# Kernel optimization log

Hardware: AMD Instinct MI355X
Metric: run time of the kernel (lower is better)

## Reference

```python
import jax, jax.numpy as jnp
import numpy as np

N_NODES = 100000
N_EDGES = 1600000
IN_CH = 6
EDGE_FEAT = 8


def glorot(key, shape):
    lim = np.sqrt(6.0 / (shape[0] + shape[1]))
    return jax.random.uniform(key, shape, jnp.float32, -lim, lim)


def setup_inputs() -> dict:
    key = jax.random.key(0)
    ks = jax.random.split(key, 10)
    x = jax.random.normal(ks[0], (N_NODES, IN_CH), jnp.float32)
    edge_index = jax.random.randint(ks[1], (2, N_EDGES), 0, N_NODES, jnp.int64)
    edge_attr = jax.random.normal(ks[2], (N_EDGES, EDGE_FEAT), jnp.float32)
    return {
        "x": x,
        "edge_index": edge_index,
        "edge_attr": edge_attr,
        "W1": glorot(ks[3], (IN_CH, 32)), "b1": jnp.zeros((32,), jnp.float32),
        "W2": glorot(ks[4], (32, 16)), "b2": jnp.zeros((16,), jnp.float32),
        "W3": glorot(ks[5], (16 * 2 + EDGE_FEAT, 32)), "b3": jnp.zeros((32,), jnp.float32),
        "W4": glorot(ks[6], (32, 1)), "b4": jnp.zeros((1,), jnp.float32),
    }


def gcn_conv(x, src, dst, W, b, n_nodes):
    # PyG GCNConv: add self-loops, symmetric deg^{-1/2} normalization,
    # linear transform, scatter-add aggregation over incoming edges, bias.
    h = x @ W  # [N, out]
    deg = jnp.zeros((n_nodes,), h.dtype).at[dst].add(1.0) + 1.0  # +1 self-loop
    dinv = jax.lax.rsqrt(deg)  # [N]
    norm = dinv[src] * dinv[dst]  # [E]
    msg = h[src] * norm[:, None]  # gather + scale
    agg = jnp.zeros_like(h).at[dst].add(msg)
    agg = agg + h * (dinv * dinv)[:, None]  # self-loop term
    return agg + b


def reference(x, edge_index, edge_attr, W1, b1, W2, b2, W3, b3, W4, b4):
    src, dst = edge_index[0], edge_index[1]
    n = x.shape[0]
    h = jax.nn.relu(gcn_conv(x, src, dst, W1, b1, n))
    h = jax.nn.relu(gcn_conv(h, src, dst, W2, b2, n))
    # edge gather-concat-MLP
    edge_input = jnp.concatenate([h[src], h[dst], edge_attr], axis=1)  # [E, 40]
    out = jax.nn.relu(edge_input @ W3 + b3) @ W4 + b4  # [E, 1]
    return out.squeeze(-1)
```

## Files before the change

### kernel.cpp

```cpp
#include <hip/hip_runtime.h>


constexpr int TPB = 256;
constexpr int NB = 256;
constexpr int BSH = 8;
constexpr int MAXB = 1024;
constexpr int EDGE_ITERS = 4;

using short8  = __attribute__((ext_vector_type(8))) short;
using f32x4   = __attribute__((ext_vector_type(4))) float;
using uintx4  = __attribute__((ext_vector_type(4))) unsigned;
using floatx4 = __attribute__((ext_vector_type(4))) float;

__device__ __forceinline__ void nt_store4(uint4 v, uint4* p) {
    uintx4 e = {v.x, v.y, v.z, v.w};
    __builtin_nontemporal_store(e, reinterpret_cast<uintx4*>(p));
}
__device__ __forceinline__ float4 nt_load_f4(const float4* p) {
    floatx4 e = __builtin_nontemporal_load(reinterpret_cast<const floatx4*>(p));
    return float4{e.x, e.y, e.z, e.w};
}

__device__ __forceinline__ float bf_lo(unsigned w) {
    return __builtin_bit_cast(float, (unsigned)(w << 16));
}
__device__ __forceinline__ float bf_hi(unsigned w) {
    return __builtin_bit_cast(float, w & 0xFFFF0000u);
}
__device__ __forceinline__ unsigned bf1(float f) {
    unsigned u = __builtin_bit_cast(unsigned, f);
    return (u + 0x7FFFu + ((u >> 16) & 1u)) >> 16;
}
__device__ __forceinline__ unsigned pk(float lo, float hi) {
    return bf1(lo) | (bf1(hi) << 16);
}
__device__ __forceinline__ void unp8(uint4 v, float* o) {
    o[0] = bf_lo(v.x); o[1] = bf_hi(v.x); o[2] = bf_lo(v.y); o[3] = bf_hi(v.y);
    o[4] = bf_lo(v.z); o[5] = bf_hi(v.z); o[6] = bf_lo(v.w); o[7] = bf_hi(v.w);
}
__device__ __forceinline__ void unp6(uint4 v, float* o) {
    o[0] = bf_lo(v.x); o[1] = bf_hi(v.x); o[2] = bf_lo(v.y); o[3] = bf_hi(v.y);
    o[4] = bf_lo(v.z); o[5] = bf_hi(v.z);
}

__global__ void k_bhist(const int* __restrict__ dst, unsigned* __restrict__ histG,
                        int E, int B, int CH) {
    __shared__ unsigned h[MAXB];
    for (int t = threadIdx.x; t < B; t += blockDim.x) h[t] = 0;
    __syncthreads();
    int b = blockIdx.x;
    int beg = b * CH, end = min(E, beg + CH);
    for (int i = beg + threadIdx.x; i < end; i += blockDim.x)
        atomicAdd(&h[__builtin_nontemporal_load(dst + i) >> BSH], 1u);
    __syncthreads();
    for (int t = threadIdx.x; t < B; t += blockDim.x) histG[b * B + t] = h[t];
}

__global__ void k_scan1t(const unsigned* __restrict__ histG, unsigned* __restrict__ bsum,
                         int M, int B) {
    __shared__ unsigned s[TPB];
    int tid = threadIdx.x;
    int i = blockIdx.x * TPB + tid;
    unsigned v = (i < M) ? histG[(i % NB) * B + (i / NB)] : 0u;
    s[tid] = v;
    __syncthreads();
    for (int ofs = TPB / 2; ofs > 0; ofs >>= 1) {
        if (tid < ofs) s[tid] += s[tid + ofs];
        __syncthreads();
    }
    if (tid == 0) bsum[blockIdx.x] = s[0];
}

__global__ void k_scan2(unsigned* __restrict__ bsum, int nb) {
    __shared__ unsigned s[512];
    int tid = threadIdx.x;
    unsigned v = (tid < nb) ? bsum[tid] : 0u;
    s[tid] = v;
    __syncthreads();
    for (int ofs = 1; ofs < 512; ofs <<= 1) {
        unsigned t = (tid >= ofs) ? s[tid - ofs] : 0u;
        __syncthreads();
        s[tid] += t;
        __syncthreads();
    }
    if (tid < nb) bsum[tid] = s[tid] - v;
}

__global__ void k_scan3t(const unsigned* __restrict__ histG, const unsigned* __restrict__ bsum,
                         unsigned* __restrict__ scannedM, int M, int B) {
    __shared__ unsigned s[TPB];
    int tid = threadIdx.x;
    int i = blockIdx.x * TPB + tid;
    unsigned v = (i < M) ? histG[(i % NB) * B + (i / NB)] : 0u;
    s[tid] = v;
    __syncthreads();
    for (int ofs = 1; ofs < TPB; ofs <<= 1) {
        unsigned t = (tid >= ofs) ? s[tid - ofs] : 0u;
        __syncthreads();
        s[tid] += t;
        __syncthreads();
    }
    if (i < M) scannedM[i] = bsum[blockIdx.x] + s[tid] - v;
}

__global__ void k_bscatter(const int* __restrict__ src, const int* __restrict__ dst,
                           const unsigned* __restrict__ scannedM, unsigned* __restrict__ lvl1,
                           int E, int B, int CH) {
    __shared__ unsigned cur[MAXB];
    int b = blockIdx.x;
    for (int t = threadIdx.x; t < B; t += blockDim.x) cur[t] = scannedM[t * NB + b];
    __syncthreads();
    int beg = b * CH, end = min(E, beg + CH);
    for (int i = beg + threadIdx.x; i < end; i += blockDim.x) {
        int d = __builtin_nontemporal_load(dst + i);
        int sv = __builtin_nontemporal_load(src + i);
        int bk = d >> BSH;
        unsigned p = atomicAdd(&cur[bk], 1u);
        lvl1[p] = ((unsigned)sv << BSH) | (unsigned)(d & ((1 << BSH) - 1));
    }
}

__global__ void k_bbuild(const unsigned* __restrict__ lvl1, const unsigned* __restrict__ scannedM,
                         const float* __restrict__ x, unsigned* __restrict__ rowptr,
                         float* __restrict__ dinv, uint4* __restrict__ xs,
                         int* __restrict__ csr_src, int N, int E, int B) {
    __shared__ unsigned cnt[1 << BSH];
    __shared__ unsigned ro[1 << BSH];
    int b = blockIdx.x;
    int tid = threadIdx.x;
    unsigned gbase = scannedM[(size_t)b * NB];
    unsigned gend = (b + 1 < B) ? scannedM[(size_t)(b + 1) * NB] : (unsigned)E;
    cnt[tid] = 0;
    __syncthreads();
    for (unsigned i = gbase + tid; i < gend; i += (unsigned)blockDim.x)
        atomicAdd(&cnt[lvl1[i] & ((1u << BSH) - 1u)], 1u);
    __syncthreads();
    unsigned v = cnt[tid];
    ro[tid] = v;
    __syncthreads();
    for (int ofs = 1; ofs < (1 << BSH); ofs <<= 1) {
        unsigned t = (tid >= ofs) ? ro[tid - ofs] : 0u;
        __syncthreads();
        ro[tid] += t;
        __syncthreads();
    }
    unsigned excl = ro[tid] - v;
    int n = (b << BSH) + tid;
    if (n < N) {
        rowptr[n] = gbase + excl;
        float di = rsqrtf((float)v + 1.0f);
        dinv[n] = di;
        const float* xr = x + (size_t)n * 6;
        uint4 o;
        o.x = pk(xr[0] * di, xr[1] * di);
        o.y = pk(xr[2] * di, xr[3] * di);
        o.z = pk(xr[4] * di, xr[5] * di);
        o.w = 0u;
        xs[n] = o;
        if (n == N - 1) rowptr[N] = gend;
    }
    __syncthreads();
    cnt[tid] = gbase + excl;
    __syncthreads();
    for (unsigned i = gbase + tid; i < gend; i += (unsigned)blockDim.x) {
        unsigned w = lvl1[i];
        unsigned p = atomicAdd(&cnt[w & ((1u << BSH) - 1u)], 1u);
        csr_src[p] = (int)(w >> BSH);
    }
}

__global__ void k_gagg6f(const unsigned* __restrict__ rowptr, const int* __restrict__ csr_src,
                         const float* __restrict__ dinv, const uint4* __restrict__ xs,
                         const float* __restrict__ W1, const float* __restrict__ b1,
                         const float* __restrict__ W2, uint4* __restrict__ hs2, int N) {
    int gid = blockIdx.x * blockDim.x + threadIdx.x;
    int n = gid >> 2, q = gid & 3;
    if (n >= N) return;
    unsigned beg = rowptr[n], end = rowptr[n + 1];
    float acc[6] = {0.f, 0.f, 0.f, 0.f, 0.f, 0.f};
    for (unsigned j = beg + q; j < end; j += 4) {
        int s = __builtin_nontemporal_load(csr_src + j);
        float t[6];
        unp6(xs[s], t);
#pragma unroll
        for (int i = 0; i < 6; ++i) acc[i] += t[i];
    }
#pragma unroll
    for (int i = 0; i < 6; ++i) {
        acc[i] += __shfl_xor(acc[i], 1);
        acc[i] += __shfl_xor(acc[i], 2);
    }
    float t6[6];
    unp6(xs[n], t6);
#pragma unroll
    for (int i = 0; i < 6; ++i) acc[i] += t6[i];
    float di = dinv[n];
    float h1[8];
#pragma unroll
    for (int cc = 0; cc < 8; ++cc) {
        int oc = q * 8 + cc;
        float s = 0.f;
#pragma unroll
        for (int k = 0; k < 6; ++k) s = fmaf(acc[k], W1[k * 32 + oc], s);
        h1[cc] = fmaxf(fmaf(s, di, b1[oc]), 0.f);
    }
    float z[16];
#pragma unroll
    for (int j = 0; j < 16; ++j) z[j] = 0.f;
#pragma unroll
    for (int cc = 0; cc < 8; ++cc) {
        int c = q * 8 + cc;
        float a = h1[cc];
#pragma unroll
        for (int j = 0; j < 16; ++j) z[j] = fmaf(a, W2[c * 16 + j], z[j]);
    }
#pragma unroll
    for (int j = 0; j < 16; ++j) {
        z[j] += __shfl_xor(z[j], 1);
        z[j] += __shfl_xor(z[j], 2);
    }
    if (q < 2) {
        unsigned w[4];
#pragma unroll
        for (int p = 0; p < 4; ++p)
            w[p] = pk(z[q * 8 + 2 * p] * di, z[q * 8 + 2 * p + 1] * di);
        nt_store4(uint4{w[0], w[1], w[2], w[3]}, hs2 + (size_t)n * 2 + q);
    }
}

__global__ void k_gagg16(const unsigned* __restrict__ rowptr, const int* __restrict__ csr_src,
                         const float* __restrict__ dinv, const uint4* __restrict__ hs2,
                         const float* __restrict__ b2, uint4* __restrict__ h2, int N) {
    int gid = blockIdx.x * blockDim.x + threadIdx.x;
    int n = gid >> 3, q = gid & 7;
    int h = q & 1, e4 = q >> 1;
    if (n >= N) return;
    unsigned beg = rowptr[n], end = rowptr[n + 1];
    float acc[8] = {0.f, 0.f, 0.f, 0.f, 0.f, 0.f, 0.f, 0.f};
    for (unsigned j = beg + e4; j < end; j += 4) {
        int s = __builtin_nontemporal_load(csr_src + j);
        float t[8];
        unp8(hs2[(size_t)s * 2 + h], t);
#pragma unroll
        for (int i = 0; i < 8; ++i) acc[i] += t[i];
    }
#pragma unroll
    for (int i = 0; i < 8; ++i) {
        acc[i] += __shfl_xor(acc[i], 2);
        acc[i] += __shfl_xor(acc[i], 4);
    }
    if (e4) return;
    float t8[8];
    unp8(hs2[(size_t)n * 2 + h], t8);
    float di = dinv[n];
    unsigned w[4];
#pragma unroll
    for (int i = 0; i < 4; ++i) {
        float r0 = fmaxf(fmaf(acc[2 * i] + t8[2 * i], di, b2[h * 8 + 2 * i]), 0.f);
        float r1 = fmaxf(fmaf(acc[2 * i + 1] + t8[2 * i + 1], di, b2[h * 8 + 2 * i + 1]), 0.f);
        w[i] = pk(r0, r1);
    }
    h2[(size_t)n * 2 + h] = uint4{w[0], w[1], w[2], w[3]};
}

__global__ void k_wprep(const float* __restrict__ W3, const float* __restrict__ b3,
                        uint4* __restrict__ w3tab) {
    int lane = threadIdx.x;
    if (lane >= 64) return;
    int l15 = lane & 15, kb = lane >> 4;
    unsigned w0[2][4], w1[2][4];
#pragma unroll
    for (int t = 0; t < 2; ++t) {
#pragma unroll
        for (int p = 0; p < 4; ++p) {
            int k0 = kb * 8 + 2 * p;
            w0[t][p] = pk(W3[k0 * 32 + t * 16 + l15], W3[(k0 + 1) * 32 + t * 16 + l15]);
            int k1 = 32 + kb * 8 + 2 * p;
            float f0 = (k1 < 40) ? W3[k1 * 32 + t * 16 + l15]
                                 : (k1 == 40 ? b3[t * 16 + l15] : 0.f);
            float f1 = (k1 + 1 < 40) ? W3[(k1 + 1) * 32 + t * 16 + l15] : 0.f;
            w1[t][p] = pk(f0, f1);
        }
    }
    w3tab[lane * 4 + 0] = uint4{w0[0][0], w0[0][1], w0[0][2], w0[0][3]};
    w3tab[lane * 4 + 1] = uint4{w0[1][0], w0[1][1], w0[1][2], w0[1][3]};
    w3tab[lane * 4 + 2] = uint4{w1[0][0], w1[0][1], w1[0][2], w1[0][3]};
    w3tab[lane * 4 + 3] = uint4{w1[1][0], w1[1][1], w1[1][2], w1[1][3]};
}

__global__ void __launch_bounds__(TPB) k_edge_mfma(
    const int* __restrict__ src, const int* __restrict__ dst,
    const uint4* __restrict__ h2, const float* __restrict__ eattr,
    const uint4* __restrict__ w3tab, const float* __restrict__ W4,
    const float* __restrict__ b4, float* __restrict__ out, int E) {
    const int lane = threadIdx.x & 63;
    const int wave = threadIdx.x >> 6;
    const int l15 = lane & 15;
    const int kb = lane >> 4;

    short8 w3k0[2], w3k1[2];
    {
        const uint4* wt = w3tab + (size_t)lane * 4;
        w3k0[0] = __builtin_bit_cast(short8, wt[0]);
        w3k0[1] = __builtin_bit_cast(short8, wt[1]);
        w3k1[0] = __builtin_bit_cast(short8, wt[2]);
        w3k1[1] = __builtin_bit_cast(short8, wt[3]);
    }
    const float4 w4v0 = reinterpret_cast<const float4*>(W4)[kb];
    const float4 w4v1 = reinterpret_cast<const float4*>(W4)[4 + kb];
    const float b4v = b4[0];
    const int* idx_tab = (kb >= 2) ? dst : src;
    const long base0 = ((long)blockIdx.x * 4 + wave) * (16L * EDGE_ITERS);

    const uint4 one_u = (kb == 1) ? uint4{0x3F80u, 0u, 0u, 0u} : uint4{0u, 0u, 0u, 0u};
    const short8 one_s8 = __builtin_bit_cast(short8, one_u);

    auto eclamp = [&](int it) -> size_t {
        long et = base0 + (long)it * 16 + l15;
        return (size_t)(et < E ? et : (long)(E - 1));
    };
    auto load_a1 = [&](int it) -> short8 {
        if (kb != 0) return one_s8;
        const float4* ea = reinterpret_cast<const float4*>(eattr + eclamp(it) * 8);
        float4 e0 = nt_load_f4(ea);
        float4 e1 = nt_load_f4(ea + 1);
        return __builtin_bit_cast(short8, uint4{pk(e0.x, e0.y), pk(e0.z, e0.w),
                                                pk(e1.x, e1.y), pk(e1.z, e1.w)});
    };

    int idx[EDGE_ITERS];
#pragma unroll
    for (int it = 0; it < EDGE_ITERS; ++it)
        idx[it] = __builtin_nontemporal_load(idx_tab + eclamp(it));

    uint4 hvA = h2[(size_t)idx[0] * 2 + (kb & 1)];
    short8 a1A = load_a1(0);
    uint4 hvB = h2[(size_t)idx[1] * 2 + (kb & 1)];
    short8 a1B = load_a1(1);

#pragma unroll
    for (int it = 0; it < EDGE_ITERS; ++it) {
        uint4 hvC{0u, 0u, 0u, 0u};
        short8 a1C = one_s8;
        if (it + 2 < EDGE_ITERS) {
            hvC = h2[(size_t)idx[it + 2] * 2 + (kb & 1)];
            a1C = load_a1(it + 2);
        }

        short8 a0 = __builtin_bit_cast(short8, hvA);
        f32x4 c0 = {0.f, 0.f, 0.f, 0.f}, c1 = {0.f, 0.f, 0.f, 0.f};
        c0 = __builtin_amdgcn_mfma_f32_16x16x32_bf16(w3k0[0], a0, c0, 0, 0, 0);
        c0 = __builtin_amdgcn_mfma_f32_16x16x32_bf16(w3k1[0], a1A, c0, 0, 0, 0);
        c1 = __builtin_amdgcn_mfma_f32_16x16x32_bf16(w3k0[1], a0, c1, 0, 0, 0);
        c1 = __builtin_amdgcn_mfma_f32_16x16x32_bf16(w3k1[1], a1A, c1, 0, 0, 0);

        float z = fmaxf(c0[0], 0.f) * w4v0.x;
        z = fmaf(fmaxf(c0[1], 0.f), w4v0.y, z);
        z = fmaf(fmaxf(c0[2], 0.f), w4v0.z, z);
        z = fmaf(fmaxf(c0[3], 0.f), w4v0.w, z);
        z = fmaf(fmaxf(c1[0], 0.f), w4v1.x, z);
        z = fmaf(fmaxf(c1[1], 0.f), w4v1.y, z);
        z = fmaf(fmaxf(c1[2], 0.f), w4v1.z, z);
        z = fmaf(fmaxf(c1[3], 0.f), w4v1.w, z);
        z += __shfl_xor(z, 16);
        z += __shfl_xor(z, 32);
        long erow = base0 + (long)it * 16 + l15;
        if (kb == 0 && erow < E) __builtin_nontemporal_store(z + b4v, out + erow);

        hvA = hvB; a1A = a1B;
        hvB = hvC; a1B = a1C;
    }
}

extern "C" void kernel_launch(void* const* d_in, const int* in_sizes, int n_in,
                              void* d_out, int out_size, void* d_ws, size_t ws_size,
                              hipStream_t stream) {
    const float* x     = (const float*)d_in[0];
    const int*   ei    = (const int*)d_in[1];
    const float* eattr = (const float*)d_in[2];
    const float* W1 = (const float*)d_in[3];
    const float* b1 = (const float*)d_in[4];
    const float* W2 = (const float*)d_in[5];
    const float* b2 = (const float*)d_in[6];
    const float* W3 = (const float*)d_in[7];
    const float* b3 = (const float*)d_in[8];
    const float* W4 = (const float*)d_in[9];
    const float* b4 = (const float*)d_in[10];
    float* out = (float*)d_out;

    const int N = in_sizes[0] / 6;
    const int E = in_sizes[2] / 8;
    const int* src = ei;
    const int* dst = ei + E;

    const int B  = (N + (1 << BSH) - 1) >> BSH;
    const int CH = (E + NB - 1) / NB;
    const int M  = B * NB;
    const int nbM = (M + TPB - 1) / TPB;

    char* wsb = (char*)d_ws;
    size_t off = 0;
    auto alloc4 = [&](size_t elems) {
        void* p = wsb + off;
        off += ((elems * 4 + 15) & ~(size_t)15);
        return p;
    };
    unsigned* rowptr   = (unsigned*)alloc4(N + 1);
    float*    dinv     = (float*)alloc4(N);
    unsigned* bsum     = (unsigned*)alloc4(512);
    unsigned* histG    = (unsigned*)alloc4((size_t)NB * B);
    unsigned* scannedM = (unsigned*)alloc4((size_t)NB * B);
    int*      csr_src  = (int*)alloc4(E);
    unsigned* big      = (unsigned*)alloc4((size_t)N * 16 > (size_t)E ? (size_t)N * 16 : (size_t)E);
    uint4*    xs       = (uint4*)alloc4((size_t)N * 4);
    uint4*    w3tab    = (uint4*)alloc4(64 * 4 * 4);

    unsigned* lvl1 = big;
    uint4*    hs2  = (uint4*)big;
    uint4*    h2   = (uint4*)(big + (size_t)N * 8);

    k_wprep<<<1, 64, 0, stream>>>(W3, b3, w3tab);

    k_bhist   <<<NB, TPB, 0, stream>>>(dst, histG, E, B, CH);
    k_scan1t  <<<nbM, TPB, 0, stream>>>(histG, bsum, M, B);
    k_scan2   <<<1, 512, 0, stream>>>(bsum, nbM);
    k_scan3t  <<<nbM, TPB, 0, stream>>>(histG, bsum, scannedM, M, B);
    k_bscatter<<<NB, TPB, 0, stream>>>(src, dst, scannedM, lvl1, E, B, CH);
    k_bbuild  <<<B, 1 << BSH, 0, stream>>>(lvl1, scannedM, x, rowptr, dinv, xs, csr_src, N, E, B);

    k_gagg6f<<<((size_t)N * 4 + TPB - 1) / TPB, TPB, 0, stream>>>(
        rowptr, csr_src, dinv, xs, W1, b1, W2, hs2, N);

    k_gagg16<<<((size_t)N * 8 + TPB - 1) / TPB, TPB, 0, stream>>>(
        rowptr, csr_src, dinv, hs2, b2, h2, N);

    const long per_block = 4L * 16 * EDGE_ITERS;
    const int eblocks = (int)((E + per_block - 1) / per_block);
    k_edge_mfma<<<eblocks, TPB, 0, stream>>>(src, dst, (const uint4*)h2, eattr,
                                             (const uint4*)w3tab, W4, b4, out, E);
}
```

Baseline: 178.2 us.

## Switch edge MLP to 32x32x16 MFMA processing 32 edges per wave

Reworks the edge MLP so each wave handles 32 edges per iteration with three 32x32x16 bf16 MFMAs (src features, dst features, edge attrs plus bias) instead of four 16x16x32 MFMAs over 16 edges. The weight table is repacked into three K-slices per lane, and the W4 reduction now needs only one cross-lane shuffle. This halves the number of blocks, amortises index and weight setup over more edges and cuts shuffles. In exchange each lane issues two gathers per iteration (src and dst) and holds a 16-wide accumulator, which raises register pressure.

```diff
diff --git a/kernel.cpp b/kernel.cpp
--- a/kernel.cpp
+++ b/kernel.cpp
@@ -8,7 +8,7 @@
 constexpr int EDGE_ITERS = 4;
 
 using short8  = __attribute__((ext_vector_type(8))) short;
-using f32x4   = __attribute__((ext_vector_type(4))) float;
+using f32x16  = __attribute__((ext_vector_type(16))) float;
 using uintx4  = __attribute__((ext_vector_type(4))) unsigned;
 using floatx4 = __attribute__((ext_vector_type(4))) float;
 
@@ -267,25 +267,19 @@
                         uint4* __restrict__ w3tab) {
     int lane = threadIdx.x;
     if (lane >= 64) return;
-    int l15 = lane & 15, kb = lane >> 4;
-    unsigned w0[2][4], w1[2][4];
-#pragma unroll
-    for (int t = 0; t < 2; ++t) {
+    int j = lane & 31, hi = lane >> 5;
+#pragma unroll
+    for (int s = 0; s < 3; ++s) {
+        unsigned w[4];
 #pragma unroll
         for (int p = 0; p < 4; ++p) {
-            int k0 = kb * 8 + 2 * p;
-            w0[t][p] = pk(W3[k0 * 32 + t * 16 + l15], W3[(k0 + 1) * 32 + t * 16 + l15]);
-            int k1 = 32 + kb * 8 + 2 * p;
-            float f0 = (k1 < 40) ? W3[k1 * 32 + t * 16 + l15]
-                                 : (k1 == 40 ? b3[t * 16 + l15] : 0.f);
-            float f1 = (k1 + 1 < 40) ? W3[(k1 + 1) * 32 + t * 16 + l15] : 0.f;
-            w1[t][p] = pk(f0, f1);
+            int k0 = s * 16 + hi * 8 + 2 * p;
+            float f0 = (k0 < 40) ? W3[k0 * 32 + j] : (k0 == 40 ? b3[j] : 0.f);
+            float f1 = (k0 + 1 < 40) ? W3[(k0 + 1) * 32 + j] : 0.f;
+            w[p] = pk(f0, f1);
         }
-    }
-    w3tab[lane * 4 + 0] = uint4{w0[0][0], w0[0][1], w0[0][2], w0[0][3]};
-    w3tab[lane * 4 + 1] = uint4{w0[1][0], w0[1][1], w0[1][2], w0[1][3]};
-    w3tab[lane * 4 + 2] = uint4{w1[0][0], w1[0][1], w1[0][2], w1[0][3]};
-    w3tab[lane * 4 + 3] = uint4{w1[1][0], w1[1][1], w1[1][2], w1[1][3]};
+        w3tab[lane * 3 + s] = uint4{w[0], w[1], w[2], w[3]};
+    }
 }
 
 __global__ void __launch_bounds__(TPB) k_edge_mfma(
@@ -295,32 +289,30 @@
     const float* __restrict__ b4, float* __restrict__ out, int E) {
     const int lane = threadIdx.x & 63;
     const int wave = threadIdx.x >> 6;
-    const int l15 = lane & 15;
-    const int kb = lane >> 4;
-
-    short8 w3k0[2], w3k1[2];
+    const int e31 = lane & 31;
+    const int hi = lane >> 5;
+
+    short8 wA0, wA1, wA2;
     {
-        const uint4* wt = w3tab + (size_t)lane * 4;
-        w3k0[0] = __builtin_bit_cast(short8, wt[0]);
-        w3k0[1] = __builtin_bit_cast(short8, wt[1]);
-        w3k1[0] = __builtin_bit_cast(short8, wt[2]);
-        w3k1[1] = __builtin_bit_cast(short8, wt[3]);
-    }
-    const float4 w4v0 = reinterpret_cast<const float4*>(W4)[kb];
-    const float4 w4v1 = reinterpret_cast<const float4*>(W4)[4 + kb];
+        const uint4* wt = w3tab + (size_t)lane * 3;
+        wA0 = __builtin_bit_cast(short8, wt[0]);
+        wA1 = __builtin_bit_cast(short8, wt[1]);
+        wA2 = __builtin_bit_cast(short8, wt[2]);
+    }
+    const float4* W4v = reinterpret_cast<const float4*>(W4);
+    const float4 w4q0 = W4v[hi], w4q1 = W4v[2 + hi], w4q2 = W4v[4 + hi], w4q3 = W4v[6 + hi];
     const float b4v = b4[0];
-    const int* idx_tab = (kb >= 2) ? dst : src;
-    const long base0 = ((long)blockIdx.x * 4 + wave) * (16L * EDGE_ITERS);
-
-    const uint4 one_u = (kb == 1) ? uint4{0x3F80u, 0u, 0u, 0u} : uint4{0u, 0u, 0u, 0u};
+    const long base0 = ((long)blockIdx.x * 4 + wave) * (32L * EDGE_ITERS);
+
+    const uint4 one_u = (hi == 1) ? uint4{0x3F80u, 0u, 0u, 0u} : uint4{0u, 0u, 0u, 0u};
     const short8 one_s8 = __builtin_bit_cast(short8, one_u);
 
     auto eclamp = [&](int it) -> size_t {
-        long et = base0 + (long)it * 16 + l15;
+        long et = base0 + (long)it * 32 + e31;
         return (size_t)(et < E ? et : (long)(E - 1));
     };
-    auto load_a1 = [&](int it) -> short8 {
-        if (kb != 0) return one_s8;
+    auto load_a2 = [&](int it) -> short8 {
+        if (hi != 0) return one_s8;
         const float4* ea = reinterpret_cast<const float4*>(eattr + eclamp(it) * 8);
         float4 e0 = nt_load_f4(ea);
         float4 e1 = nt_load_f4(ea + 1);
@@ -328,47 +320,49 @@
                                                 pk(e1.x, e1.y), pk(e1.z, e1.w)});
     };
 
-    int idx[EDGE_ITERS];
-#pragma unroll
-    for (int it = 0; it < EDGE_ITERS; ++it)
-        idx[it] = __builtin_nontemporal_load(idx_tab + eclamp(it));
-
-    uint4 hvA = h2[(size_t)idx[0] * 2 + (kb & 1)];
-    short8 a1A = load_a1(0);
-    uint4 hvB = h2[(size_t)idx[1] * 2 + (kb & 1)];
-    short8 a1B = load_a1(1);
-
+    int is[EDGE_ITERS], id[EDGE_ITERS];
 #pragma unroll
     for (int it = 0; it < EDGE_ITERS; ++it) {
-        uint4 hvC{0u, 0u, 0u, 0u};
-        short8 a1C = one_s8;
+        is[it] = __builtin_nontemporal_load(src + eclamp(it));
+        id[it] = __builtin_nontemporal_load(dst + eclamp(it));
+    }
+
+    uint4 hsA = h2[(size_t)is[0] * 2 + hi], hdA = h2[(size_t)id[0] * 2 + hi];
+    short8 a2A = load_a2(0);
+    uint4 hsB = h2[(size_t)is[1] * 2 + hi], hdB = h2[(size_t)id[1] * 2 + hi];
+    short8 a2B = load_a2(1);
+
+#pragma unroll
+    for (int it = 0; it < EDGE_ITERS; ++it) {
+        uint4 hsC{0u, 0u, 0u, 0u}, hdC{0u, 0u, 0u, 0u};
+        short8 a2C = one_s8;
         if (it + 2 < EDGE_ITERS) {
-            hvC = h2[(size_t)idx[it + 2] * 2 + (kb & 1)];
-            a1C = load_a1(it + 2);
+            hsC = h2[(size_t)is[it + 2] * 2 + hi];
+            hdC = h2[(size_t)id[it + 2] * 2 + hi];
+            a2C = load_a2(it + 2);
         }
 
-        short8 a0 = __builtin_bit_cast(short8, hvA);
-        f32x4 c0 = {0.f, 0.f, 0.f, 0.f}, c1 = {0.f, 0.f, 0.f, 0.f};
-        c0 = __builtin_amdgcn_mfma_f32_16x16x32_bf16(w3k0[0], a0, c0, 0, 0, 0);
-        c0 = __builtin_amdgcn_mfma_f32_16x16x32_bf16(w3k1[0], a1A, c0, 0, 0, 0);
-        c1 = __builtin_amdgcn_mfma_f32_16x16x32_bf16(w3k0[1], a0, c1, 0, 0, 0);
-        c1 = __builtin_amdgcn_mfma_f32_16x16x32_bf16(w3k1[1], a1A, c1, 0, 0, 0);
-
-        float z = fmaxf(c0[0], 0.f) * w4v0.x;
-        z = fmaf(fmaxf(c0[1], 0.f), w4v0.y, z);
-        z = fmaf(fmaxf(c0[2], 0.f), w4v0.z, z);
-        z = fmaf(fmaxf(c0[3], 0.f), w4v0.w, z);
-        z = fmaf(fmaxf(c1[0], 0.f), w4v1.x, z);
-        z = fmaf(fmaxf(c1[1], 0.f), w4v1.y, z);
-        z = fmaf(fmaxf(c1[2], 0.f), w4v1.z, z);
-        z = fmaf(fmaxf(c1[3], 0.f), w4v1.w, z);
-        z += __shfl_xor(z, 16);
+        f32x16 c;
+#pragma unroll
+        for (int i = 0; i < 16; ++i) c[i] = 0.f;
+        c = __builtin_amdgcn_mfma_f32_32x32x16_bf16(wA0, __builtin_bit_cast(short8, hsA), c, 0, 0, 0);
+        c = __builtin_amdgcn_mfma_f32_32x32x16_bf16(wA1, __builtin_bit_cast(short8, hdA), c, 0, 0, 0);
+        c = __builtin_amdgcn_mfma_f32_32x32x16_bf16(wA2, a2A, c, 0, 0, 0);
+
+        float z = 0.f;
+#pragma unroll
+        for (int r = 0; r < 4; ++r) {
+            z = fmaf(fmaxf(c[0 * 4 + r], 0.f), ((const float*)&w4q0)[r], z);
+            z = fmaf(fmaxf(c[1 * 4 + r], 0.f), ((const float*)&w4q1)[r], z);
+            z = fmaf(fmaxf(c[2 * 4 + r], 0.f), ((const float*)&w4q2)[r], z);
+            z = fmaf(fmaxf(c[3 * 4 + r], 0.f), ((const float*)&w4q3)[r], z);
+        }
         z += __shfl_xor(z, 32);
-        long erow = base0 + (long)it * 16 + l15;
-        if (kb == 0 && erow < E) __builtin_nontemporal_store(z + b4v, out + erow);
-
-        hvA = hvB; a1A = a1B;
-        hvB = hvC; a1B = a1C;
+        long erow = base0 + (long)it * 32 + e31;
+        if (hi == 0 && erow < E) __builtin_nontemporal_store(z + b4v, out + erow);
+
+        hsA = hsB; hdA = hdB; a2A = a2B;
+        hsB = hsC; hdB = hdC; a2B = a2C;
     }
 }
 
@@ -413,7 +407,7 @@
     int*      csr_src  = (int*)alloc4(E);
     unsigned* big      = (unsigned*)alloc4((size_t)N * 16 > (size_t)E ? (size_t)N * 16 : (size_t)E);
     uint4*    xs       = (uint4*)alloc4((size_t)N * 4);
-    uint4*    w3tab    = (uint4*)alloc4(64 * 4 * 4);
+    uint4*    w3tab    = (uint4*)alloc4(64 * 3 * 4);
 
     unsigned* lvl1 = big;
     uint4*    hs2  = (uint4*)big;
@@ -434,7 +428,7 @@
     k_gagg16<<<((size_t)N * 8 + TPB - 1) / TPB, TPB, 0, stream>>>(
         rowptr, csr_src, dinv, hs2, b2, h2, N);
 
-    const long per_block = 4L * 16 * EDGE_ITERS;
+    const long per_block = 4L * 32 * EDGE_ITERS;
     const int eblocks = (int)((E + per_block - 1) / per_block);
     k_edge_mfma<<<eblocks, TPB, 0, stream>>>(src, dst, (const uint4*)h2, eattr,
                                              (const uint4*)w3tab, W4, b4, out, E);
```

Measured after the change: 172.3 us. -3.3%, faster.
